# Performance work log

Hardware: AMD Instinct MI355X
Metric: run time of the kernel (lower is better)

The kernel has to match this reference:

```python
import jax, jax.numpy as jnp
import numpy as np

B, L = 1, 320
CS, CZ, CH, H, PQ, PV = 384, 128, 16, 12, 4, 8
INF, EPS = 1e5, 1e-8


def _quat_to_rot(q):
    w, x, y, z = q[..., 0], q[..., 1], q[..., 2], q[..., 3]
    r0 = jnp.stack([1 - 2*(y*y + z*z), 2*(x*y - w*z), 2*(x*z + w*y)], -1)
    r1 = jnp.stack([2*(x*y + w*z), 1 - 2*(x*x + z*z), 2*(y*z - w*x)], -1)
    r2 = jnp.stack([2*(x*z - w*y), 2*(y*z + w*x), 1 - 2*(x*x + y*y)], -1)
    return jnp.stack([r0, r1, r2], -2)


def setup_inputs():
    key = jax.random.key(0)
    ks = jax.random.split(key, 12)

    def lin(k, fan_in, fan_out):
        k1, k2 = jax.random.split(k)
        lim = 1.0 / np.sqrt(fan_in)
        return (jax.random.uniform(k1, (fan_in, fan_out), minval=-lim, maxval=lim, dtype=jnp.float32),
                jax.random.uniform(k2, (fan_out,), minval=-lim, maxval=lim, dtype=jnp.float32))

    s = jax.random.normal(ks[0], (B, L, CS), dtype=jnp.float32)
    quat = jax.random.normal(ks[1], (B, L, 4), dtype=jnp.float32)
    quat = quat / jnp.linalg.norm(quat, axis=-1, keepdims=True)
    rot = _quat_to_rot(quat)                                   # proper rotations (B,L,3,3)
    trans = 10.0 * jax.random.normal(ks[2], (B, L, 3), dtype=jnp.float32)
    z = jax.random.normal(ks[3], (B, L, L, CZ), dtype=jnp.float32)
    frame_mask = jnp.ones((B, L), dtype=jnp.float32)

    Wq, bq = lin(ks[4], CS, CH * H)
    Wkv, bkv = lin(ks[5], CS, 2 * CH * H)
    Wqp, bqp = lin(ks[6], CS, 6 * H * PQ)
    Wkvp, bkvp = lin(ks[7], CS, 6 * H * (PQ + PV))
    Wg, bg = lin(ks[8], CS, H * PQ)
    geom_weights = jnp.ones((3,), jnp.float32)
    dir_weight = jnp.asarray(0.5, jnp.float32)
    head_weights = 0.02 * jax.random.normal(ks[9], (H,), dtype=jnp.float32)
    concat_dim = H * (CH + 7 * PV) + H * CZ                    # 2400
    Wo, bo = lin(ks[10], concat_dim, CS)
    return dict(s=s, rot=rot, trans=trans, z=z, frame_mask=frame_mask,
                Wq=Wq, bq=bq, Wkv=Wkv, bkv=bkv, Wqp=Wqp, bqp=bqp,
                Wkvp=Wkvp, bkvp=bkvp, Wg=Wg, bg=bg,
                geom_weights=geom_weights, dir_weight=dir_weight,
                head_weights=head_weights, Wo=Wo, bo=bo)


def reference(s, rot, trans, z, frame_mask, Wq, bq, Wkv, bkv, Wqp, bqp,
              Wkvp, bkvp, Wg, bg, geom_weights, dir_weight, head_weights, Wo, bo):
    def proc_pts(pts_flat, P):
        # (B,L,6*H*P) -> rotate coords+translate, rotate dirs -> (B,L,H,P,6)
        pts = pts_flat.reshape(B, L, H, P, 6)
        coords = jnp.einsum('blij,blhpj->blhpi', rot, pts[..., :3]) + trans[:, :, None, None, :]
        dirs = jnp.einsum('blij,blhpj->blhpi', rot, pts[..., 3:])
        return jnp.concatenate([coords, dirs], -1)

    q = (s @ Wq + bq).reshape(B, L, H, CH)
    kv = s @ Wkv + bkv
    k = kv[..., :CH * H].reshape(B, L, H, CH)
    v = kv[..., CH * H:].reshape(B, L, H, CH)

    q_pts = proc_pts(s @ Wqp + bqp, PQ)
    kv_pts = s @ Wkvp + bkvp
    k_pts = proc_pts(kv_pts[..., :6 * H * PQ], PQ)
    v_pts = proc_pts(kv_pts[..., 6 * H * PQ:], PV)

    gate = jax.nn.sigmoid(s @ Wg + bg).reshape(B, L, H, PQ, 1)
    q_pts = q_pts * gate

    scalar_att = jnp.einsum('bqhc,bkhc->bhqk', q, k) / np.sqrt(CH).astype(np.float32)

    # position attention: per-pair point distances + log + inverse, mean over points
    delta = q_pts[:, :, None, :, :, :3] - k_pts[:, None, :, :, :, :3]   # (B,Lq,Lk,H,PQ,3)
    d = jnp.linalg.norm(delta, axis=-1)
    pos_att = (d + jnp.log(d + EPS) + 1.0 / (d + EPS)).mean(-1).transpose(0, 3, 1, 2)

    # direction attention: per-point dot minus cross-product 'curvature'
    qd, kd = q_pts[..., 3:], k_pts[..., 3:]
    dot = jnp.einsum('bqhpd,bkhpd->bqkhp', qd, kd)                       # (B,Lq,Lk,H,P)
    cr = jnp.cross(qd[:, :, None, :, None, :, :], kd[:, None, :, :, :, None, :])  # (B,Lq,Lk,H,Pk,Pq,3)
    cross = jnp.linalg.norm(cr, axis=-1).mean(-1)                        # (B,Lq,Lk,H,Pk)
    nq = jnp.linalg.norm(qd, axis=-1)[:, :, None]                        # (B,Lq,1,H,P)
    nk = jnp.linalg.norm(kd, axis=-1)[:, None]                           # (B,1,Lk,H,P)
    dir_att = (dot - cross / (nq * nk + EPS)).mean(-1).transpose(0, 3, 1, 2)

    att = scalar_att + dir_weight * (geom_weights[0] * pos_att + geom_weights[1] * dir_att)
    att = att * head_weights[:, None, None]
    mask2d = frame_mask[:, None, None, :] * frame_mask[:, None, :, None]  # (B,1,L,L)
    att = jax.nn.softmax(att + INF * (mask2d - 1.0), axis=-1)

    o_scalar = jnp.einsum('bhqk,bkhc->bqhc', att, v)
    o_geom = jnp.einsum('bhqk,bkhpd->bqhpd', att, v_pts)                 # (B,L,H,PV,6)

    # map aggregated geometry back into local frames
    rotT = jnp.swapaxes(rot, -1, -2)
    trans_inv = -jnp.einsum('blij,blj->bli', rotT, trans)
    lc = jnp.einsum('blij,blhpj->blhpi', rotT, o_geom[..., :3]) + trans_inv[:, :, None, None, :]
    ld = jnp.einsum('blij,blhpj->blhpi', rotT, o_geom[..., 3:6])
    ld = ld / jnp.maximum(jnp.linalg.norm(ld, axis=-1, keepdims=True), 1e-12)  # F.normalize
    ln = jnp.linalg.norm(lc, axis=-1, keepdims=True)
    o_geom7 = jnp.concatenate([lc, ld, ln], -1)                          # (B,L,H,PV,7)

    o_pair = jnp.einsum('bhij,bijk->bihk', att, z)                       # (B,L,H,CZ)
    out = jnp.concatenate([o_scalar.reshape(B, L, H * CH),
                           o_geom7.reshape(B, L, H * PV * 7),
                           o_pair.reshape(B, L, H * CZ)], -1)
    return out @ Wo + bo
```

## Files before the change

### kernel.cpp

```cpp
#include <hip/hip_runtime.h>
#include <hip/hip_bf16.h>
#include <math.h>

#define LSEQ 320
#define CS 384
#define CZ 128
#define CH 16
#define NH 12
#define PQ 4
#define PV 8
#define EPSF 1e-8f

typedef short short8 __attribute__((ext_vector_type(8)));
typedef float f32x4 __attribute__((ext_vector_type(4)));
typedef unsigned short ush2 __attribute__((ext_vector_type(2)));

__device__ __forceinline__ unsigned short f2b(float x) {
    union { float f; unsigned u; } v; v.f = x;
    unsigned r = (v.u + 0x7FFF + ((v.u >> 16) & 1)) >> 16;
    return (unsigned short)r;
}
__device__ __forceinline__ float b2f(unsigned short h) {
    union { unsigned u; float f; } v; v.u = ((unsigned)h) << 16;
    return v.f;
}

#define OFF_Q       0
#define OFF_KV      61440
#define OFF_QPT     184320
#define OFF_ATTHI   552960
#define OFF_ATTLO   1372160
#define OFF_CCHI    2191360
#define OFF_CCLO    2575360
#define OFF_SHI     2959360
#define OFF_SMID    2990080
#define OFF_SLO     3020800
#define OFF_WCATHI  3051520
#define OFF_WCATMID 3392512
#define OFF_WCATLO  3733504
#define OFF_BCAT    4074496
#define OFF_WOHI    4076272
#define OFF_WOLO    4537072
#define OFF_VKVHI   4997872
#define OFF_VKVLO   5120752
#define OFF_QPR     5243632
#define OFF_KVPR    5335792
#define OFF_GATE    5612272
#define OFF_PART    5627632
#define OFF_KROW    6242032

__global__ __launch_bounds__(256) void k_cast(
    const float* __restrict__ s,
    const float* __restrict__ Wq, const float* __restrict__ bq,
    const float* __restrict__ Wkv, const float* __restrict__ bkv,
    const float* __restrict__ Wqp, const float* __restrict__ bqp,
    const float* __restrict__ Wkvp, const float* __restrict__ bkvp,
    const float* __restrict__ Wg, const float* __restrict__ bg,
    const float* __restrict__ Wo,
    unsigned short* __restrict__ s_hi, unsigned short* __restrict__ s_mid,
    unsigned short* __restrict__ s_lo,
    unsigned short* __restrict__ w_hi, unsigned short* __restrict__ w_mid,
    unsigned short* __restrict__ w_lo,
    float* __restrict__ bcat,
    unsigned short* __restrict__ wo_hi, unsigned short* __restrict__ wo_lo,
    float* __restrict__ ph_hi, float* __restrict__ ph_lo)
{
    int i = blockIdx.x * 256 + threadIdx.x;
    if (i < 122880) {
        float x = s[i];
        unsigned short hi = f2b(x);
        float r1 = x - b2f(hi);
        unsigned short mid = f2b(r1);
        s_hi[i] = hi; s_mid[i] = mid; s_lo[i] = f2b(r1 - b2f(mid));
        return;
    }
    i -= 122880;
    if (i < 681984) {
        int k = i / 1776, c = i - k * 1776;
        float v;
        if (c < 192)       v = Wq[(size_t)k * 192 + c];
        else if (c < 576)  v = Wkv[(size_t)k * 384 + c - 192];
        else if (c < 864)  v = Wqp[(size_t)k * 288 + c - 576];
        else if (c < 1728) v = Wkvp[(size_t)k * 864 + c - 864];
        else               v = Wg[(size_t)k * 48 + c - 1728];
        unsigned short hi = f2b(v);
        float r1 = v - b2f(hi);
        unsigned short mid = f2b(r1);
        w_hi[i] = hi; w_mid[i] = mid; w_lo[i] = f2b(r1 - b2f(mid));
        return;
    }
    i -= 681984;
    if (i < 1776) {
        float v;
        if (i < 192)       v = bq[i];
        else if (i < 576)  v = bkv[i - 192];
        else if (i < 864)  v = bqp[i - 576];
        else if (i < 1728) v = bkvp[i - 864];
        else               v = bg[i - 1728];
        bcat[i] = v;
        return;
    }
    i -= 1776;
    if (i < 921600) {
        float v = Wo[i];
        unsigned short hi = f2b(v);
        wo_hi[i] = hi; wo_lo[i] = f2b(v - b2f(hi));
        return;
    }
    i -= 921600;
    if (i < 204800) { ph_hi[i] = 0.0f; return; }
    i -= 204800;
    if (i < 204800) ph_lo[i] = 0.0f;
}

__global__ __launch_bounds__(256) void k_proj(
    const unsigned short* __restrict__ s_hi, const unsigned short* __restrict__ s_mid,
    const unsigned short* __restrict__ s_lo,
    const unsigned short* __restrict__ wc_hi, const unsigned short* __restrict__ wc_mid,
    const unsigned short* __restrict__ wc_lo,
    const float* __restrict__ bcat,
    float* __restrict__ qo, float* __restrict__ kvo,
    float* __restrict__ qpr, float* __restrict__ kvpr, float* __restrict__ gate)
{
    __shared__ unsigned short a_h[64][56], a_m[64][56], a_l[64][56];
    __shared__ unsigned short w_h[48][56], w_m[48][56], w_l[48][56];
    int col0 = blockIdx.x * 48, l0 = blockIdx.y * 64;
    int tid = threadIdx.x;
    int lane = tid & 63, w = tid >> 6;
    int ncol = lane & 15, blk = lane >> 4, mrow = (lane >> 4) * 4;

    float* dst; int nc, cbase; bool sig = false;
    if (col0 < 192)       { nc = 192; cbase = col0;        dst = qo;   }
    else if (col0 < 576)  { nc = 384; cbase = col0 - 192;  dst = kvo;  }
    else if (col0 < 864)  { nc = 288; cbase = col0 - 576;  dst = qpr;  }
    else if (col0 < 1728) { nc = 864; cbase = col0 - 864;  dst = kvpr; }
    else                  { nc = 48;  cbase = 0;           dst = gate; sig = true; }

    f32x4 acc[3] = {};
    for (int k0 = 0; k0 < 384; k0 += 32) {
        __syncthreads();
        {
            int row = tid >> 2, seg = tid & 3;
            size_t off = (size_t)(l0 + row) * 384 + k0 + seg * 8;
            *(short8*)&a_h[row][seg * 8] = *(const short8*)(s_hi + off);
            *(short8*)&a_m[row][seg * 8] = *(const short8*)(s_mid + off);
            *(short8*)&a_l[row][seg * 8] = *(const short8*)(s_lo + off);
        }
        if (tid < 96) {
            int kk = tid / 3, coff = (tid % 3) * 16;
            size_t off = (size_t)(k0 + kk) * 1776 + col0 + coff;
            short8 h0 = *(const short8*)(wc_hi + off);
            short8 h1 = *(const short8*)(wc_hi + off + 8);
            short8 m0 = *(const short8*)(wc_mid + off);
            short8 m1 = *(const short8*)(wc_mid + off + 8);
            short8 l0v = *(const short8*)(wc_lo + off);
            short8 l1v = *(const short8*)(wc_lo + off + 8);
            #pragma unroll
            for (int i = 0; i < 8; i++) {
                w_h[coff + i][kk]     = (unsigned short)h0[i];
                w_h[coff + 8 + i][kk] = (unsigned short)h1[i];
                w_m[coff + i][kk]     = (unsigned short)m0[i];
                w_m[coff + 8 + i][kk] = (unsigned short)m1[i];
                w_l[coff + i][kk]     = (unsigned short)l0v[i];
                w_l[coff + 8 + i][kk] = (unsigned short)l1v[i];
            }
        }
        __syncthreads();
        short8 afh = *(short8*)&a_h[w * 16 + ncol][blk * 8];
        short8 afm = *(short8*)&a_m[w * 16 + ncol][blk * 8];
        short8 afl = *(short8*)&a_l[w * 16 + ncol][blk * 8];
        #pragma unroll
        for (int s3 = 0; s3 < 3; s3++) {
            short8 bfh = *(short8*)&w_h[s3 * 16 + ncol][blk * 8];
            short8 bfm = *(short8*)&w_m[s3 * 16 + ncol][blk * 8];
            short8 bfl = *(short8*)&w_l[s3 * 16 + ncol][blk * 8];
            acc[s3] = __builtin_amdgcn_mfma_f32_16x16x32_bf16(afm, bfm, acc[s3], 0, 0, 0);
            acc[s3] = __builtin_amdgcn_mfma_f32_16x16x32_bf16(afh, bfl, acc[s3], 0, 0, 0);
            acc[s3] = __builtin_amdgcn_mfma_f32_16x16x32_bf16(afl, bfh, acc[s3], 0, 0, 0);
            acc[s3] = __builtin_amdgcn_mfma_f32_16x16x32_bf16(afh, bfm, acc[s3], 0, 0, 0);
            acc[s3] = __builtin_amdgcn_mfma_f32_16x16x32_bf16(afm, bfh, acc[s3], 0, 0, 0);
            acc[s3] = __builtin_amdgcn_mfma_f32_16x16x32_bf16(afh, bfh, acc[s3], 0, 0, 0);
        }
    }
    #pragma unroll
    for (int s3 = 0; s3 < 3; s3++) {
        float bv = bcat[col0 + s3 * 16 + ncol];
        int cloc = cbase + s3 * 16 + ncol;
        #pragma unroll
        for (int r = 0; r < 4; r++) {
            float v2 = acc[s3][r] + bv;
            if (sig) v2 = 1.0f / (1.0f + expf(-v2));
            dst[(size_t)(l0 + w * 16 + mrow + r) * nc + cloc] = v2;
        }
    }
}

__global__ __launch_bounds__(256) void k_points(
    const float* __restrict__ qpr, const float* __restrict__ kvpr, const float* __restrict__ gate,
    const float* __restrict__ rot, const float* __restrict__ trans,
    const float* __restrict__ kv,
    float* __restrict__ qpt, float* __restrict__ krow,
    unsigned short* __restrict__ vkv_hi, unsigned short* __restrict__ vkv_lo)
{
    __shared__ float vsh[96][6];
    __shared__ float kp_s[48][6];
    __shared__ float kn_s[48];
    int l = blockIdx.x, t = threadIdx.x;
    const float* R = rot + l * 9;
    float tx = trans[l * 3], ty = trans[l * 3 + 1], tz = trans[l * 3 + 2];
    if (t < 192) {
        const float* src; float g = 1.0f; float* dst = nullptr; int vj = -1, kj = -1;
        if (t < 48)      { src = qpr + (size_t)l * 288 + t * 6; g = gate[l * 48 + t]; dst = qpt + ((size_t)l * 48 + t) * 6; }
        else if (t < 96) { kj = t - 48; src = kvpr + (size_t)l * 864 + kj * 6; }
        else             { int j = t - 96; src = kvpr + (size_t)l * 864 + 288 + j * 6; vj = j; }
        float px = src[0], py = src[1], pz = src[2], ux = src[3], uy = src[4], uz = src[5];
        float c0 = R[0] * px + R[1] * py + R[2] * pz + tx;
        float c1 = R[3] * px + R[4] * py + R[5] * pz + ty;
        float c2 = R[6] * px + R[7] * py + R[8] * pz + tz;
        float d0 = R[0] * ux + R[1] * uy + R[2] * uz;
        float d1 = R[3] * ux + R[4] * uy + R[5] * uz;
        float d2 = R[6] * ux + R[7] * uy + R[8] * uz;
        if (vj >= 0) {
            vsh[vj][0] = c0; vsh[vj][1] = c1; vsh[vj][2] = c2;
            vsh[vj][3] = d0; vsh[vj][4] = d1; vsh[vj][5] = d2;
        } else if (kj >= 0) {
            kp_s[kj][0] = c0; kp_s[kj][1] = c1; kp_s[kj][2] = c2;
            kp_s[kj][3] = d0; kp_s[kj][4] = d1; kp_s[kj][5] = d2;
            kn_s[kj] = sqrtf(d0 * d0 + d1 * d1 + d2 * d2);
        } else {
            dst[0] = c0 * g; dst[1] = c1 * g; dst[2] = c2 * g;
            dst[3] = d0 * g; dst[4] = d1 * g; dst[5] = d2 * g;
        }
    }
    __syncthreads();
    #pragma unroll
    for (int e = 0; e < 3; e++) {
        int u = t * 3 + e;
        int h = u >> 6, n = u & 63;
        float val;
        if (n < 16) val = kv[(size_t)l * 384 + 192 + h * 16 + n];
        else        val = vsh[h * 8 + (n - 16) / 6][(n - 16) % 6];
        unsigned short hi = f2b(val);
        size_t idx = ((size_t)h * 64 + n) * 320 + l;
        vkv_hi[idx] = hi;
        vkv_lo[idx] = f2b(val - b2f(hi));
    }
    for (int idx = t; idx < 576; idx += 256) {
        int h = idx / 48, j = idx - h * 48;
        float v;
        if (j < 24)      v = kp_s[h * 4 + j / 6][j % 6];
        else if (j < 40) v = kv[(size_t)l * 384 + h * 16 + (j - 24)];
        else if (j < 44) v = kn_s[h * 4 + (j - 40)];
        else             v = 0.0f;
        krow[((size_t)h * 320 + l) * 48 + j] = v;
    }
}

__global__ __launch_bounds__(256) void k_att(
    const float* __restrict__ qb, const float* __restrict__ qpt,
    const float* __restrict__ krow,
    const float* __restrict__ fm, const float* __restrict__ gw,
    const float* __restrict__ dwp, const float* __restrict__ hwp,
    unsigned short* __restrict__ att_hi, unsigned short* __restrict__ att_lo)
{
    int tid = threadIdx.x;
    int w = tid >> 6, lane = tid & 63;
    int iq = blockIdx.x * 4 + w;
    int h = blockIdx.y;

    float qv[CH];
    #pragma unroll
    for (int c = 0; c < CH; c++) qv[c] = qb[(size_t)iq * 192 + h * CH + c];
    float qp[24];
    #pragma unroll
    for (int j = 0; j < 24; j++) qp[j] = qpt[(size_t)iq * 288 + h * 24 + j];
    float nq[PQ], nq2[PQ];
    #pragma unroll
    for (int p = 0; p < PQ; p++) {
        float x = qp[p * 6 + 3], y = qp[p * 6 + 4], zz = qp[p * 6 + 5];
        nq2[p] = x * x + y * y + zz * zz;
        nq[p] = sqrtf(nq2[p]);
    }
    float dwv = dwp[0], g0 = gw[0], g1 = gw[1], hwv = hwp[h];
    float fmi = fm[iq];

    float lg[5];
    #pragma unroll
    for (int r = 0; r < 5; r++) {
        int kk = r * 64 + lane;
        const float* row = krow + ((size_t)h * 320 + kk) * 48;

        float scalar = 0.f;
        #pragma unroll
        for (int c = 0; c < CH; c++) scalar += qv[c] * row[24 + c];
        scalar *= 0.25f;

        float pos = 0.f;
        #pragma unroll
        for (int p = 0; p < PQ; p++) {
            float dx = qp[p * 6] - row[p * 6];
            float dy = qp[p * 6 + 1] - row[p * 6 + 1];
            float dz = qp[p * 6 + 2] - row[p * 6 + 2];
            float d = __builtin_amdgcn_sqrtf(dx * dx + dy * dy + dz * dz);
            float de = d + EPSF;
            pos += d + __logf(de) + __builtin_amdgcn_rcpf(de);
        }
        pos *= 0.25f;

        float dir = 0.f;
        #pragma unroll
        for (int p = 0; p < PQ; p++) {
            float kx = row[p * 6 + 3], ky = row[p * 6 + 4], kz = row[p * 6 + 5];
            float nk = row[40 + p];
            float nk2 = nk * nk;
            float cm = 0.f, dself = 0.f;
            #pragma unroll
            for (int pq = 0; pq < PQ; pq++) {
                float dq = qp[pq * 6 + 3] * kx + qp[pq * 6 + 4] * ky + qp[pq * 6 + 5] * kz;
                if (pq == p) dself = dq;
                cm += __builtin_amdgcn_sqrtf(fmaxf(nq2[pq] * nk2 - dq * dq, 0.0f));
            }
            cm *= 0.25f;
            dir += dself - cm * __builtin_amdgcn_rcpf(nq[p] * nk + EPSF);
        }
        dir *= 0.25f;

        float logit = scalar + dwv * (g0 * pos + g1 * dir);
        logit *= hwv;
        logit += 100000.0f * (fmi * fm[kk] - 1.0f);
        lg[r] = logit;
    }

    float mx = lg[0];
    #pragma unroll
    for (int r = 1; r < 5; r++) mx = fmaxf(mx, lg[r]);
    for (int m = 32; m; m >>= 1) mx = fmaxf(mx, __shfl_xor(mx, m, 64));

    float e[5], sm = 0.f;
    #pragma unroll
    for (int r = 0; r < 5; r++) { e[r] = __expf(lg[r] - mx); sm += e[r]; }
    for (int m = 32; m; m >>= 1) sm += __shfl_xor(sm, m, 64);
    float inv = 1.0f / sm;
    #pragma unroll
    for (int r = 0; r < 5; r++) {
        float p = e[r] * inv;
        unsigned short hi = f2b(p);
        size_t idx = ((size_t)h * 320 + iq) * 320 + r * 64 + lane;
        att_hi[idx] = hi;
        att_lo[idx] = f2b(p - b2f(hi));
    }
}

__global__ __launch_bounds__(256) void k_sv(
    const unsigned short* __restrict__ att_hi, const unsigned short* __restrict__ att_lo,
    const unsigned short* __restrict__ vkv_hi, const unsigned short* __restrict__ vkv_lo,
    const float* __restrict__ rot, const float* __restrict__ trans,
    unsigned short* __restrict__ cc_hi, unsigned short* __restrict__ cc_lo)
{
    __shared__ unsigned short a_hi[16][56];
    __shared__ unsigned short a_lo[16][56];
    __shared__ unsigned short bt_hi[64][56];
    __shared__ unsigned short bt_lo[64][56];
    __shared__ float ogsh[16][49];
    int iq0 = blockIdx.x * 16, h = blockIdx.y;
    int tid = threadIdx.x;
    int lane = tid & 63, w = tid >> 6;
    int ncol = lane & 15, mrow = (lane >> 4) * 4, blk = lane >> 4;

    f32x4 acc = {};
    for (int k0 = 0; k0 < 320; k0 += 32) {
        __syncthreads();
        if (tid < 64) {
            int row = tid >> 2, seg = tid & 3;
            size_t off = ((size_t)h * 320 + iq0 + row) * 320 + k0 + seg * 8;
            *(short8*)&a_hi[row][seg * 8] = *(const short8*)(att_hi + off);
            *(short8*)&a_lo[row][seg * 8] = *(const short8*)(att_lo + off);
        }
        {
            int row = tid >> 2, seg = tid & 3;
            size_t off = ((size_t)h * 64 + row) * 320 + k0 + seg * 8;
            *(short8*)&bt_hi[row][seg * 8] = *(const short8*)(vkv_hi + off);
            *(short8*)&bt_lo[row][seg * 8] = *(const short8*)(vkv_lo + off);
        }
        __syncthreads();
        short8 afh = *(short8*)&a_hi[ncol][blk * 8];
        short8 afl = *(short8*)&a_lo[ncol][blk * 8];
        short8 bfh = *(short8*)&bt_hi[w * 16 + ncol][blk * 8];
        short8 bfl = *(short8*)&bt_lo[w * 16 + ncol][blk * 8];
        acc = __builtin_amdgcn_mfma_f32_16x16x32_bf16(afh, bfh, acc, 0, 0, 0);
        acc = __builtin_amdgcn_mfma_f32_16x16x32_bf16(afh, bfl, acc, 0, 0, 0);
        acc = __builtin_amdgcn_mfma_f32_16x16x32_bf16(afl, bfh, acc, 0, 0, 0);
    }
    {
        int n = w * 16 + ncol;
        #pragma unroll
        for (int r = 0; r < 4; r++) {
            int iq = iq0 + mrow + r;
            float v = acc[r];
            if (n < 16) {
                unsigned short hi = f2b(v);
                size_t idx = (size_t)iq * 2400 + h * 16 + n;
                cc_hi[idx] = hi;
                cc_lo[idx] = f2b(v - b2f(hi));
            } else {
                ogsh[mrow + r][n - 16] = v;
            }
        }
    }
    __syncthreads();
    if (tid < 128) {
        int iqr = tid >> 3, p = tid & 7;
        int l = iq0 + iqr;
        const float* R = rot + l * 9;
        float tx = trans[l * 3], ty = trans[l * 3 + 1], tz = trans[l * 3 + 2];
        const float* o = &ogsh[iqr][p * 6];
        float gx = o[0] - tx, gy = o[1] - ty, gz = o[2] - tz;
        float l0 = R[0] * gx + R[3] * gy + R[6] * gz;
        float l1 = R[1] * gx + R[4] * gy + R[7] * gz;
        float l2 = R[2] * gx + R[5] * gy + R[8] * gz;
        float dx = o[3], dy = o[4], dz = o[5];
        float e0 = R[0] * dx + R[3] * dy + R[6] * dz;
        float e1 = R[1] * dx + R[4] * dy + R[7] * dz;
        float e2 = R[2] * dx + R[5] * dy + R[8] * dz;
        float n = sqrtf(e0 * e0 + e1 * e1 + e2 * e2);
        float inv = 1.0f / fmaxf(n, 1e-12f);
        float ln = sqrtf(l0 * l0 + l1 * l1 + l2 * l2);
        float vals[7] = { l0, l1, l2, e0 * inv, e1 * inv, e2 * inv, ln };
        size_t base = (size_t)l * 2400 + 192 + (h * PV + p) * 7;
        #pragma unroll
        for (int j = 0; j < 7; j++) {
            unsigned short hi = f2b(vals[j]);
            cc_hi[base + j] = hi;
            cc_lo[base + j] = f2b(vals[j] - b2f(hi));
        }
    }
}

__global__ __launch_bounds__(256) void k_pair(
    const unsigned short* __restrict__ att_hi, const unsigned short* __restrict__ att_lo,
    const float* __restrict__ z,
    unsigned short* __restrict__ cc_hi, unsigned short* __restrict__ cc_lo)
{
    __shared__ unsigned short a_hi[16][56];
    __shared__ unsigned short a_lo[16][56];
    __shared__ unsigned short zt_sh[128][56];
    int iq = blockIdx.x;
    int tid = threadIdx.x;
    int lane = tid & 63, w = tid >> 6;
    int ncol = lane & 15, blk = lane >> 4, mrow = (lane >> 4) * 4;

    f32x4 acc[2] = {};
    for (int k0 = 0; k0 < 320; k0 += 32) {
        __syncthreads();
        if (tid < 64) {
            int row = tid >> 2, seg = tid & 3;
            size_t off = (size_t)row * 102400 + (size_t)iq * 320 + k0 + seg * 8;
            *(short8*)&a_hi[row][seg * 8] = *(const short8*)(att_hi + off);
            *(short8*)&a_lo[row][seg * 8] = *(const short8*)(att_lo + off);
        }
        {
            int kp2 = (tid >> 4) * 2;
            int cb = (tid & 15) * 8;
            const float* src0 = z + ((size_t)iq * 320 + k0 + kp2) * 128 + cb;
            float4 a0 = *(const float4*)(src0);
            float4 a1 = *(const float4*)(src0 + 4);
            float4 b0 = *(const float4*)(src0 + 128);
            float4 b1 = *(const float4*)(src0 + 132);
            float va[8] = {a0.x, a0.y, a0.z, a0.w, a1.x, a1.y, a1.z, a1.w};
            float vb[8] = {b0.x, b0.y, b0.z, b0.w, b1.x, b1.y, b1.z, b1.w};
            #pragma unroll
            for (int c = 0; c < 8; c++) {
                ush2 pr;
                pr[0] = f2b(va[c]);
                pr[1] = f2b(vb[c]);
                *(ush2*)&zt_sh[cb + c][kp2] = pr;
            }
        }
        __syncthreads();
        short8 afh = *(short8*)&a_hi[ncol][blk * 8];
        short8 afl = *(short8*)&a_lo[ncol][blk * 8];
        #pragma unroll
        for (int s2 = 0; s2 < 2; s2++) {
            short8 bf = *(short8*)&zt_sh[w * 32 + s2 * 16 + ncol][blk * 8];
            acc[s2] = __builtin_amdgcn_mfma_f32_16x16x32_bf16(afl, bf, acc[s2], 0, 0, 0);
            acc[s2] = __builtin_amdgcn_mfma_f32_16x16x32_bf16(afh, bf, acc[s2], 0, 0, 0);
        }
    }
    #pragma unroll
    for (int s2 = 0; s2 < 2; s2++) {
        int n = w * 32 + s2 * 16 + ncol;
        #pragma unroll
        for (int r = 0; r < 4; r++) {
            int h = mrow + r;
            if (h < 12) {
                float v = acc[s2][r];
                unsigned short hi = f2b(v);
                size_t idx = (size_t)iq * 2400 + 864 + h * 128 + n;
                cc_hi[idx] = hi;
                cc_lo[idx] = f2b(v - b2f(hi));
            }
        }
    }
}

__global__ __launch_bounds__(256) void k_gemm(
    const unsigned short* __restrict__ cc_hi, const unsigned short* __restrict__ cc_lo,
    const unsigned short* __restrict__ wo_hi, const unsigned short* __restrict__ wo_lo,
    float* __restrict__ part)
{
    __shared__ unsigned short a_hi[64][56];
    __shared__ unsigned short a_lo[64][56];
    __shared__ unsigned short w_hi[48][56];
    __shared__ unsigned short w_lo[48][56];
    int iq0 = blockIdx.x * 64, col0 = blockIdx.y * 48, ks = blockIdx.z;
    int tid = threadIdx.x;
    int lane = tid & 63, w = tid >> 6;
    int ncol = lane & 15, blk = lane >> 4, mrow = (lane >> 4) * 4;

    f32x4 acc[3] = {};
    for (int kc = 0; kc < 15; kc++) {
        int k0 = ks * 480 + kc * 32;
        __syncthreads();
        {
            int row = tid >> 2, seg = tid & 3;
            size_t off = (size_t)(iq0 + row) * 2400 + k0 + seg * 8;
            *(short8*)&a_hi[row][seg * 8] = *(const short8*)(cc_hi + off);
            *(short8*)&a_lo[row][seg * 8] = *(const short8*)(cc_lo + off);
        }
        if (tid < 96) {
            int kk = tid / 3, coff = (tid % 3) * 16;
            size_t off = (size_t)(k0 + kk) * 384 + col0 + coff;
            short8 h0 = *(const short8*)(wo_hi + off);
            short8 h1 = *(const short8*)(wo_hi + off + 8);
            short8 l0v = *(const short8*)(wo_lo + off);
            short8 l1v = *(const short8*)(wo_lo + off + 8);
            #pragma unroll
            for (int i = 0; i < 8; i++) {
                w_hi[coff + i][kk]     = (unsigned short)h0[i];
                w_hi[coff + 8 + i][kk] = (unsigned short)h1[i];
                w_lo[coff + i][kk]     = (unsigned short)l0v[i];
                w_lo[coff + 8 + i][kk] = (unsigned short)l1v[i];
            }
        }
        __syncthreads();
        short8 afh = *(short8*)&a_hi[w * 16 + ncol][blk * 8];
        short8 afl = *(short8*)&a_lo[w * 16 + ncol][blk * 8];
        #pragma unroll
        for (int s3 = 0; s3 < 3; s3++) {
            short8 bfh = *(short8*)&w_hi[s3 * 16 + ncol][blk * 8];
            short8 bfl = *(short8*)&w_lo[s3 * 16 + ncol][blk * 8];
            acc[s3] = __builtin_amdgcn_mfma_f32_16x16x32_bf16(afh, bfh, acc[s3], 0, 0, 0);
            acc[s3] = __builtin_amdgcn_mfma_f32_16x16x32_bf16(afh, bfl, acc[s3], 0, 0, 0);
            acc[s3] = __builtin_amdgcn_mfma_f32_16x16x32_bf16(afl, bfh, acc[s3], 0, 0, 0);
        }
    }
    #pragma unroll
    for (int s3 = 0; s3 < 3; s3++) {
        int cn = col0 + s3 * 16 + ncol;
        #pragma unroll
        for (int r = 0; r < 4; r++)
            part[((size_t)ks * 320 + iq0 + w * 16 + mrow + r) * 384 + cn] = acc[s3][r];
    }
}

__global__ __launch_bounds__(256) void k_reduce(
    const float* __restrict__ part, const float* __restrict__ bo, float* __restrict__ out)
{
    int i = blockIdx.x * 256 + threadIdx.x;
    float v = bo[i % CS];
    #pragma unroll
    for (int ks = 0; ks < 5; ks++) v += part[(size_t)ks * 122880 + i];
    out[i] = v;
}

extern "C" void kernel_launch(void* const* d_in, const int* in_sizes, int n_in,
                              void* d_out, int out_size, void* d_ws, size_t ws_size,
                              hipStream_t stream)
{
    const float* s     = (const float*)d_in[0];
    const float* rot   = (const float*)d_in[1];
    const float* trans = (const float*)d_in[2];
    const float* z     = (const float*)d_in[3];
    const float* fm    = (const float*)d_in[4];
    const float* Wq    = (const float*)d_in[5];
    const float* bq    = (const float*)d_in[6];
    const float* Wkv   = (const float*)d_in[7];
    const float* bkv   = (const float*)d_in[8];
    const float* Wqp   = (const float*)d_in[9];
    const float* bqp   = (const float*)d_in[10];
    const float* Wkvp  = (const float*)d_in[11];
    const float* bkvp  = (const float*)d_in[12];
    const float* Wg    = (const float*)d_in[13];
    const float* bg    = (const float*)d_in[14];
    const float* gw    = (const float*)d_in[15];
    const float* dw    = (const float*)d_in[16];
    const float* hw    = (const float*)d_in[17];
    const float* Wo    = (const float*)d_in[18];
    const float* bo    = (const float*)d_in[19];

    float* ws = (float*)d_ws;
    float*          q       = ws + OFF_Q;
    float*          kv      = ws + OFF_KV;
    float*          qpt     = ws + OFF_QPT;
    unsigned short* att_hi  = (unsigned short*)(ws + OFF_ATTHI);
    unsigned short* att_lo  = (unsigned short*)(ws + OFF_ATTLO);
    float*          ph_hi   = ws + OFF_ATTHI + 12 * 51200;
    float*          ph_lo   = ws + OFF_ATTLO + 12 * 51200;
    unsigned short* cc_hi   = (unsigned short*)(ws + OFF_CCHI);
    unsigned short* cc_lo   = (unsigned short*)(ws + OFF_CCLO);
    unsigned short* s_hi    = (unsigned short*)(ws + OFF_SHI);
    unsigned short* s_mid   = (unsigned short*)(ws + OFF_SMID);
    unsigned short* s_lo    = (unsigned short*)(ws + OFF_SLO);
    unsigned short* wc_hi   = (unsigned short*)(ws + OFF_WCATHI);
    unsigned short* wc_mid  = (unsigned short*)(ws + OFF_WCATMID);
    unsigned short* wc_lo   = (unsigned short*)(ws + OFF_WCATLO);
    float*          bcat    = ws + OFF_BCAT;
    unsigned short* wo_hi   = (unsigned short*)(ws + OFF_WOHI);
    unsigned short* wo_lo   = (unsigned short*)(ws + OFF_WOLO);
    unsigned short* vkv_hi  = (unsigned short*)(ws + OFF_VKVHI);
    unsigned short* vkv_lo  = (unsigned short*)(ws + OFF_VKVLO);
    float*          qpr     = ws + OFF_QPR;
    float*          kvpr    = ws + OFF_KVPR;
    float*          gate    = ws + OFF_GATE;
    float*          part    = ws + OFF_PART;
    float*          krow    = ws + OFF_KROW;
    float* out = (float*)d_out;

    k_cast<<<dim3(8352), dim3(256), 0, stream>>>(s, Wq, bq, Wkv, bkv, Wqp, bqp,
                                                 Wkvp, bkvp, Wg, bg, Wo,
                                                 s_hi, s_mid, s_lo, wc_hi, wc_mid, wc_lo,
                                                 bcat, wo_hi, wo_lo, ph_hi, ph_lo);
    k_proj<<<dim3(37, 5), dim3(256), 0, stream>>>(s_hi, s_mid, s_lo, wc_hi, wc_mid, wc_lo,
                                                  bcat, q, kv, qpr, kvpr, gate);
    k_points<<<dim3(LSEQ), dim3(256), 0, stream>>>(qpr, kvpr, gate, rot, trans, kv,
                                                   qpt, krow, vkv_hi, vkv_lo);
    k_att<<<dim3(80, NH), dim3(256), 0, stream>>>(q, qpt, krow, fm, gw, dw, hw,
                                                  att_hi, att_lo);
    k_sv<<<dim3(20, NH), dim3(256), 0, stream>>>(att_hi, att_lo, vkv_hi, vkv_lo,
                                                 rot, trans, cc_hi, cc_lo);
    k_pair<<<dim3(LSEQ), dim3(256), 0, stream>>>(att_hi, att_lo, z, cc_hi, cc_lo);
    k_gemm<<<dim3(5, 8, 5), dim3(256), 0, stream>>>(cc_hi, cc_lo, wo_hi, wo_lo, part);
    k_reduce<<<dim3(480), dim3(256), 0, stream>>>(part, bo, out);
}
```

Baseline: 219.1 us.

## Pre-transpose weights for vectorized LDS staging and merge sv/pair kernels

After: 216.7 us. No clear change (-1.1%).

```diff
diff --git a/kernel.cpp b/kernel.cpp
--- a/kernel.cpp
+++ b/kernel.cpp
@@ -48,6 +48,11 @@
 #define OFF_GATE    5612272
 #define OFF_PART    5627632
 #define OFF_KROW    6242032
+#define OFF_WCTHI   6426352
+#define OFF_WCTMID  6767344
+#define OFF_WCTLO   7108336
+#define OFF_WOTHI   7449328
+#define OFF_WOTLO   7910128
 
 __global__ __launch_bounds__(256) void k_cast(
     const float* __restrict__ s,
@@ -113,11 +118,45 @@
     if (i < 204800) ph_lo[i] = 0.0f;
 }
 
+__global__ __launch_bounds__(256) void k_tr(
+    const unsigned short* __restrict__ wc_hi, const unsigned short* __restrict__ wc_mid,
+    const unsigned short* __restrict__ wc_lo,
+    const unsigned short* __restrict__ wo_hi, const unsigned short* __restrict__ wo_lo,
+    unsigned short* __restrict__ wcT_hi, unsigned short* __restrict__ wcT_mid,
+    unsigned short* __restrict__ wcT_lo,
+    unsigned short* __restrict__ woT_hi, unsigned short* __restrict__ woT_lo)
+{
+    int m = blockIdx.z;
+    const unsigned short* in; unsigned short* outp; int R, C;
+    if (m == 0)      { in = wc_hi;  outp = wcT_hi;  R = 384;  C = 1776; }
+    else if (m == 1) { in = wc_mid; outp = wcT_mid; R = 384;  C = 1776; }
+    else if (m == 2) { in = wc_lo;  outp = wcT_lo;  R = 384;  C = 1776; }
+    else if (m == 3) { in = wo_hi;  outp = woT_hi;  R = 2400; C = 384;  }
+    else             { in = wo_lo;  outp = woT_lo;  R = 2400; C = 384;  }
+    int r0 = blockIdx.x * 64, c0 = blockIdx.y * 64;
+    if (r0 >= R || c0 >= C) return;
+    __shared__ unsigned short t[64][65];
+    int tid = threadIdx.x;
+    #pragma unroll
+    for (int rep = 0; rep < 16; rep++) {
+        int idx = rep * 256 + tid;
+        int i = idx >> 6, j = idx & 63;
+        if (r0 + i < R && c0 + j < C) t[i][j] = in[(size_t)(r0 + i) * C + c0 + j];
+    }
+    __syncthreads();
+    #pragma unroll
+    for (int rep = 0; rep < 16; rep++) {
+        int idx = rep * 256 + tid;
+        int i = idx >> 6, j = idx & 63;
+        if (c0 + i < C && r0 + j < R) outp[(size_t)(c0 + i) * R + r0 + j] = t[j][i];
+    }
+}
+
 __global__ __launch_bounds__(256) void k_proj(
     const unsigned short* __restrict__ s_hi, const unsigned short* __restrict__ s_mid,
     const unsigned short* __restrict__ s_lo,
-    const unsigned short* __restrict__ wc_hi, const unsigned short* __restrict__ wc_mid,
-    const unsigned short* __restrict__ wc_lo,
+    const unsigned short* __restrict__ wcT_hi, const unsigned short* __restrict__ wcT_mid,
+    const unsigned short* __restrict__ wcT_lo,
     const float* __restrict__ bcat,
     float* __restrict__ qo, float* __restrict__ kvo,
     float* __restrict__ qpr, float* __restrict__ kvpr, float* __restrict__ gate)
@@ -146,24 +185,12 @@
             *(short8*)&a_m[row][seg * 8] = *(const short8*)(s_mid + off);
             *(short8*)&a_l[row][seg * 8] = *(const short8*)(s_lo + off);
         }
-        if (tid < 96) {
-            int kk = tid / 3, coff = (tid % 3) * 16;
-            size_t off = (size_t)(k0 + kk) * 1776 + col0 + coff;
-            short8 h0 = *(const short8*)(wc_hi + off);
-            short8 h1 = *(const short8*)(wc_hi + off + 8);
-            short8 m0 = *(const short8*)(wc_mid + off);
-            short8 m1 = *(const short8*)(wc_mid + off + 8);
-            short8 l0v = *(const short8*)(wc_lo + off);
-            short8 l1v = *(const short8*)(wc_lo + off + 8);
-            #pragma unroll
-            for (int i = 0; i < 8; i++) {
-                w_h[coff + i][kk]     = (unsigned short)h0[i];
-                w_h[coff + 8 + i][kk] = (unsigned short)h1[i];
-                w_m[coff + i][kk]     = (unsigned short)m0[i];
-                w_m[coff + 8 + i][kk] = (unsigned short)m1[i];
-                w_l[coff + i][kk]     = (unsigned short)l0v[i];
-                w_l[coff + 8 + i][kk] = (unsigned short)l1v[i];
-            }
+        if (tid < 192) {
+            int row = tid >> 2, seg = tid & 3;
+            size_t off = (size_t)(col0 + row) * 384 + k0 + seg * 8;
+            *(short8*)&w_h[row][seg * 8] = *(const short8*)(wcT_hi + off);
+            *(short8*)&w_m[row][seg * 8] = *(const short8*)(wcT_mid + off);
+            *(short8*)&w_l[row][seg * 8] = *(const short8*)(wcT_lo + off);
         }
         __syncthreads();
         short8 afh = *(short8*)&a_h[w * 16 + ncol][blk * 8];
@@ -351,153 +378,143 @@
     }
 }
 
-__global__ __launch_bounds__(256) void k_sv(
+__global__ __launch_bounds__(256) void k_svpair(
     const unsigned short* __restrict__ att_hi, const unsigned short* __restrict__ att_lo,
     const unsigned short* __restrict__ vkv_hi, const unsigned short* __restrict__ vkv_lo,
+    const float* __restrict__ z,
     const float* __restrict__ rot, const float* __restrict__ trans,
     unsigned short* __restrict__ cc_hi, unsigned short* __restrict__ cc_lo)
 {
     __shared__ unsigned short a_hi[16][56];
     __shared__ unsigned short a_lo[16][56];
-    __shared__ unsigned short bt_hi[64][56];
-    __shared__ unsigned short bt_lo[64][56];
+    __shared__ unsigned short B[128][56];
     __shared__ float ogsh[16][49];
-    int iq0 = blockIdx.x * 16, h = blockIdx.y;
-    int tid = threadIdx.x;
-    int lane = tid & 63, w = tid >> 6;
-    int ncol = lane & 15, mrow = (lane >> 4) * 4, blk = lane >> 4;
-
-    f32x4 acc = {};
-    for (int k0 = 0; k0 < 320; k0 += 32) {
-        __syncthreads();
-        if (tid < 64) {
-            int row = tid >> 2, seg = tid & 3;
-            size_t off = ((size_t)h * 320 + iq0 + row) * 320 + k0 + seg * 8;
-            *(short8*)&a_hi[row][seg * 8] = *(const short8*)(att_hi + off);
-            *(short8*)&a_lo[row][seg * 8] = *(const short8*)(att_lo + off);
-        }
-        {
-            int row = tid >> 2, seg = tid & 3;
-            size_t off = ((size_t)h * 64 + row) * 320 + k0 + seg * 8;
-            *(short8*)&bt_hi[row][seg * 8] = *(const short8*)(vkv_hi + off);
-            *(short8*)&bt_lo[row][seg * 8] = *(const short8*)(vkv_lo + off);
-        }
-        __syncthreads();
-        short8 afh = *(short8*)&a_hi[ncol][blk * 8];
-        short8 afl = *(short8*)&a_lo[ncol][blk * 8];
-        short8 bfh = *(short8*)&bt_hi[w * 16 + ncol][blk * 8];
-        short8 bfl = *(short8*)&bt_lo[w * 16 + ncol][blk * 8];
-        acc = __builtin_amdgcn_mfma_f32_16x16x32_bf16(afh, bfh, acc, 0, 0, 0);
-        acc = __builtin_amdgcn_mfma_f32_16x16x32_bf16(afh, bfl, acc, 0, 0, 0);
-        acc = __builtin_amdgcn_mfma_f32_16x16x32_bf16(afl, bfh, acc, 0, 0, 0);
-    }
-    {
-        int n = w * 16 + ncol;
-        #pragma unroll
-        for (int r = 0; r < 4; r++) {
-            int iq = iq0 + mrow + r;
-            float v = acc[r];
-            if (n < 16) {
-                unsigned short hi = f2b(v);
-                size_t idx = (size_t)iq * 2400 + h * 16 + n;
-                cc_hi[idx] = hi;
-                cc_lo[idx] = f2b(v - b2f(hi));
-            } else {
-                ogsh[mrow + r][n - 16] = v;
-            }
-        }
-    }
-    __syncthreads();
-    if (tid < 128) {
-        int iqr = tid >> 3, p = tid & 7;
-        int l = iq0 + iqr;
-        const float* R = rot + l * 9;
-        float tx = trans[l * 3], ty = trans[l * 3 + 1], tz = trans[l * 3 + 2];
-        const float* o = &ogsh[iqr][p * 6];
-        float gx = o[0] - tx, gy = o[1] - ty, gz = o[2] - tz;
-        float l0 = R[0] * gx + R[3] * gy + R[6] * gz;
-        float l1 = R[1] * gx + R[4] * gy + R[7] * gz;
-        float l2 = R[2] * gx + R[5] * gy + R[8] * gz;
-        float dx = o[3], dy = o[4], dz = o[5];
-        float e0 = R[0] * dx + R[3] * dy + R[6] * dz;
-        float e1 = R[1] * dx + R[4] * dy + R[7] * dz;
-        float e2 = R[2] * dx + R[5] * dy + R[8] * dz;
-        float n = sqrtf(e0 * e0 + e1 * e1 + e2 * e2);
-        float inv = 1.0f / fmaxf(n, 1e-12f);
-        float ln = sqrtf(l0 * l0 + l1 * l1 + l2 * l2);
-        float vals[7] = { l0, l1, l2, e0 * inv, e1 * inv, e2 * inv, ln };
-        size_t base = (size_t)l * 2400 + 192 + (h * PV + p) * 7;
-        #pragma unroll
-        for (int j = 0; j < 7; j++) {
-            unsigned short hi = f2b(vals[j]);
-            cc_hi[base + j] = hi;
-            cc_lo[base + j] = f2b(vals[j] - b2f(hi));
-        }
-    }
-}
-
-__global__ __launch_bounds__(256) void k_pair(
-    const unsigned short* __restrict__ att_hi, const unsigned short* __restrict__ att_lo,
-    const float* __restrict__ z,
-    unsigned short* __restrict__ cc_hi, unsigned short* __restrict__ cc_lo)
-{
-    __shared__ unsigned short a_hi[16][56];
-    __shared__ unsigned short a_lo[16][56];
-    __shared__ unsigned short zt_sh[128][56];
-    int iq = blockIdx.x;
+    int bid = blockIdx.x;
     int tid = threadIdx.x;
     int lane = tid & 63, w = tid >> 6;
     int ncol = lane & 15, blk = lane >> 4, mrow = (lane >> 4) * 4;
 
-    f32x4 acc[2] = {};
-    for (int k0 = 0; k0 < 320; k0 += 32) {
+    if (bid < 240) {
+        int iq0 = (bid % 20) * 16, h = bid / 20;
+        f32x4 acc = {};
+        for (int k0 = 0; k0 < 320; k0 += 32) {
+            __syncthreads();
+            if (tid < 64) {
+                int row = tid >> 2, seg = tid & 3;
+                size_t off = ((size_t)h * 320 + iq0 + row) * 320 + k0 + seg * 8;
+                *(short8*)&a_hi[row][seg * 8] = *(const short8*)(att_hi + off);
+                *(short8*)&a_lo[row][seg * 8] = *(const short8*)(att_lo + off);
+            }
+            {
+                int row = tid >> 2, seg = tid & 3;
+                size_t off = ((size_t)h * 64 + row) * 320 + k0 + seg * 8;
+                *(short8*)&B[row][seg * 8]      = *(const short8*)(vkv_hi + off);
+                *(short8*)&B[64 + row][seg * 8] = *(const short8*)(vkv_lo + off);
+            }
+            __syncthreads();
+            short8 afh = *(short8*)&a_hi[ncol][blk * 8];
+            short8 afl = *(short8*)&a_lo[ncol][blk * 8];
+            short8 bfh = *(short8*)&B[w * 16 + ncol][blk * 8];
+            short8 bfl = *(short8*)&B[64 + w * 16 + ncol][blk * 8];
+            acc = __builtin_amdgcn_mfma_f32_16x16x32_bf16(afh, bfh, acc, 0, 0, 0);
+            acc = __builtin_amdgcn_mfma_f32_16x16x32_bf16(afh, bfl, acc, 0, 0, 0);
+            acc = __builtin_amdgcn_mfma_f32_16x16x32_bf16(afl, bfh, acc, 0, 0, 0);
+        }
+        {
+            int n = w * 16 + ncol;
+            #pragma unroll
+            for (int r = 0; r < 4; r++) {
+                int iq = iq0 + mrow + r;
+                float v = acc[r];
+                if (n < 16) {
+                    unsigned short hi = f2b(v);
+                    size_t idx = (size_t)iq * 2400 + h * 16 + n;
+                    cc_hi[idx] = hi;
+                    cc_lo[idx] = f2b(v - b2f(hi));
+                } else {
+                    ogsh[mrow + r][n - 16] = v;
+                }
+            }
+        }
         __syncthreads();
-        if (tid < 64) {
-            int row = tid >> 2, seg = tid & 3;
-            size_t off = (size_t)row * 102400 + (size_t)iq * 320 + k0 + seg * 8;
-            *(short8*)&a_hi[row][seg * 8] = *(const short8*)(att_hi + off);
-            *(short8*)&a_lo[row][seg * 8] = *(const short8*)(att_lo + off);
-        }
-        {
-            int kp2 = (tid >> 4) * 2;
-            int cb = (tid & 15) * 8;
-            const float* src0 = z + ((size_t)iq * 320 + k0 + kp2) * 128 + cb;
-            float4 a0 = *(const float4*)(src0);
-            float4 a1 = *(const float4*)(src0 + 4);
-            float4 b0 = *(const float4*)(src0 + 128);
-            float4 b1 = *(const float4*)(src0 + 132);
-            float va[8] = {a0.x, a0.y, a0.z, a0.w, a1.x, a1.y, a1.z, a1.w};
-            float vb[8] = {b0.x, b0.y, b0.z, b0.w, b1.x, b1.y, b1.z, b1.w};
+        if (tid < 128) {
+            int iqr = tid >> 3, p = tid & 7;
+            int l = iq0 + iqr;
+            const float* R = rot + l * 9;
+            float tx = trans[l * 3], ty = trans[l * 3 + 1], tz = trans[l * 3 + 2];
+            const float* o = &ogsh[iqr][p * 6];
+            float gx = o[0] - tx, gy = o[1] - ty, gz = o[2] - tz;
+            float l0 = R[0] * gx + R[3] * gy + R[6] * gz;
+            float l1 = R[1] * gx + R[4] * gy + R[7] * gz;
+            float l2 = R[2] * gx + R[5] * gy + R[8] * gz;
+            float dx = o[3], dy = o[4], dz = o[5];
+            float e0 = R[0] * dx + R[3] * dy + R[6] * dz;
+            float e1 = R[1] * dx + R[4] * dy + R[7] * dz;
+            float e2 = R[2] * dx + R[5] * dy + R[8] * dz;
+            float n = sqrtf(e0 * e0 + e1 * e1 + e2 * e2);
+            float inv = 1.0f / fmaxf(n, 1e-12f);
+            float ln = sqrtf(l0 * l0 + l1 * l1 + l2 * l2);
+            float vals[7] = { l0, l1, l2, e0 * inv, e1 * inv, e2 * inv, ln };
+            size_t base = (size_t)l * 2400 + 192 + (h * PV + p) * 7;
             #pragma unroll
-            for (int c = 0; c < 8; c++) {
-                ush2 pr;
-                pr[0] = f2b(va[c]);
-                pr[1] = f2b(vb[c]);
-                *(ush2*)&zt_sh[cb + c][kp2] = pr;
-            }
-        }
-        __syncthreads();
-        short8 afh = *(short8*)&a_hi[ncol][blk * 8];
-        short8 afl = *(short8*)&a_lo[ncol][blk * 8];
+            for (int j = 0; j < 7; j++) {
+                unsigned short hi = f2b(vals[j]);
+                cc_hi[base + j] = hi;
+                cc_lo[base + j] = f2b(vals[j] - b2f(hi));
+            }
+        }
+    } else {
+        int iq = bid - 240;
+        f32x4 acc[2] = {};
+        for (int k0 = 0; k0 < 320; k0 += 32) {
+            __syncthreads();
+            if (tid < 64) {
+                int row = tid >> 2, seg = tid & 3;
+                size_t off = (size_t)row * 102400 + (size_t)iq * 320 + k0 + seg * 8;
+                *(short8*)&a_hi[row][seg * 8] = *(const short8*)(att_hi + off);
+                *(short8*)&a_lo[row][seg * 8] = *(const short8*)(att_lo + off);
+            }
+            {
+                int kp2 = (tid >> 4) * 2;
+                int cb = (tid & 15) * 8;
+                const float* src0 = z + ((size_t)iq * 320 + k0 + kp2) * 128 + cb;
+                float4 a0 = *(const float4*)(src0);
+                float4 a1 = *(const float4*)(src0 + 4);
+                float4 b0 = *(const float4*)(src0 + 128);
+                float4 b1 = *(const float4*)(src0 + 132);
+                float va[8] = {a0.x, a0.y, a0.z, a0.w, a1.x, a1.y, a1.z, a1.w};
+                float vb[8] = {b0.x, b0.y, b0.z, b0.w, b1.x, b1.y, b1.z, b1.w};
+                #pragma unroll
+                for (int c = 0; c < 8; c++) {
+                    ush2 pr;
+                    pr[0] = f2b(va[c]);
+                    pr[1] = f2b(vb[c]);
+                    *(ush2*)&B[cb + c][kp2] = pr;
+                }
+            }
+            __syncthreads();
+            short8 afh = *(short8*)&a_hi[ncol][blk * 8];
+            short8 afl = *(short8*)&a_lo[ncol][blk * 8];
+            #pragma unroll
+            for (int s2 = 0; s2 < 2; s2++) {
+                short8 bf = *(short8*)&B[w * 32 + s2 * 16 + ncol][blk * 8];
+                acc[s2] = __builtin_amdgcn_mfma_f32_16x16x32_bf16(afl, bf, acc[s2], 0, 0, 0);
+                acc[s2] = __builtin_amdgcn_mfma_f32_16x16x32_bf16(afh, bf, acc[s2], 0, 0, 0);
+            }
+        }
         #pragma unroll
         for (int s2 = 0; s2 < 2; s2++) {
-            short8 bf = *(short8*)&zt_sh[w * 32 + s2 * 16 + ncol][blk * 8];
-            acc[s2] = __builtin_amdgcn_mfma_f32_16x16x32_bf16(afl, bf, acc[s2], 0, 0, 0);
-            acc[s2] = __builtin_amdgcn_mfma_f32_16x16x32_bf16(afh, bf, acc[s2], 0, 0, 0);
-        }
-    }
-    #pragma unroll
-    for (int s2 = 0; s2 < 2; s2++) {
-        int n = w * 32 + s2 * 16 + ncol;
-        #pragma unroll
-        for (int r = 0; r < 4; r++) {
-            int h = mrow + r;
-            if (h < 12) {
-                float v = acc[s2][r];
-                unsigned short hi = f2b(v);
-                size_t idx = (size_t)iq * 2400 + 864 + h * 128 + n;
-                cc_hi[idx] = hi;
-                cc_lo[idx] = f2b(v - b2f(hi));
+            int n = w * 32 + s2 * 16 + ncol;
+            #pragma unroll
+            for (int r = 0; r < 4; r++) {
+                int h = mrow + r;
+                if (h < 12) {
+                    float v = acc[s2][r];
+                    unsigned short hi = f2b(v);
+                    size_t idx = (size_t)iq * 2400 + 864 + h * 128 + n;
+                    cc_hi[idx] = hi;
+                    cc_lo[idx] = f2b(v - b2f(hi));
+                }
             }
         }
     }
@@ -505,7 +522,7 @@
 
 __global__ __launch_bounds__(256) void k_gemm(
     const unsigned short* __restrict__ cc_hi, const unsigned short* __restrict__ cc_lo,
-    const unsigned short* __restrict__ wo_hi, const unsigned short* __restrict__ wo_lo,
+    const unsigned short* __restrict__ woT_hi, const unsigned short* __restrict__ woT_lo,
     float* __restrict__ part)
 {
     __shared__ unsigned short a_hi[64][56];
@@ -527,20 +544,11 @@
             *(short8*)&a_hi[row][seg * 8] = *(const short8*)(cc_hi + off);
             *(short8*)&a_lo[row][seg * 8] = *(const short8*)(cc_lo + off);
         }
-        if (tid < 96) {
-            int kk = tid / 3, coff = (tid % 3) * 16;
-            size_t off = (size_t)(k0 + kk) * 384 + col0 + coff;
-            short8 h0 = *(const short8*)(wo_hi + off);
-            short8 h1 = *(const short8*)(wo_hi + off + 8);
-            short8 l0v = *(const short8*)(wo_lo + off);
-            short8 l1v = *(const short8*)(wo_lo + off + 8);
-            #pragma unroll
-            for (int i = 0; i < 8; i++) {
-                w_hi[coff + i][kk]     = (unsigned short)h0[i];
-                w_hi[coff + 8 + i][kk] = (unsigned short)h1[i];
-                w_lo[coff + i][kk]     = (unsigned short)l0v[i];
-                w_lo[coff + 8 + i][kk] = (unsigned short)l1v[i];
-            }
+        if (tid < 192) {
+            int row = tid >> 2, seg = tid & 3;
+            size_t off = (size_t)(col0 + row) * 2400 + k0 + seg * 8;
+            *(short8*)&w_hi[row][seg * 8] = *(const short8*)(woT_hi + off);
+            *(short8*)&w_lo[row][seg * 8] = *(const short8*)(woT_lo + off);
         }
         __syncthreads();
         short8 afh = *(short8*)&a_hi[w * 16 + ncol][blk * 8];
@@ -624,21 +632,27 @@
     float*          gate    = ws + OFF_GATE;
     float*          part    = ws + OFF_PART;
     float*          krow    = ws + OFF_KROW;
+    unsigned short* wcT_hi  = (unsigned short*)(ws + OFF_WCTHI);
+    unsigned short* wcT_mid = (unsigned short*)(ws + OFF_WCTMID);
+    unsigned short* wcT_lo  = (unsigned short*)(ws + OFF_WCTLO);
+    unsigned short* woT_hi  = (unsigned short*)(ws + OFF_WOTHI);
+    unsigned short* woT_lo  = (unsigned short*)(ws + OFF_WOTLO);
     float* out = (float*)d_out;
 
     k_cast<<<dim3(8352), dim3(256), 0, stream>>>(s, Wq, bq, Wkv, bkv, Wqp, bqp,
                                                  Wkvp, bkvp, Wg, bg, Wo,
                                                  s_hi, s_mid, s_lo, wc_hi, wc_mid, wc_lo,
                                                  bcat, wo_hi, wo_lo, ph_hi, ph_lo);
-    k_proj<<<dim3(37, 5), dim3(256), 0, stream>>>(s_hi, s_mid, s_lo, wc_hi, wc_mid, wc_lo,
+    k_tr<<<dim3(38, 28, 5), dim3(256), 0, stream>>>(wc_hi, wc_mid, wc_lo, wo_hi, wo_lo,
+                                                    wcT_hi, wcT_mid, wcT_lo, woT_hi, woT_lo);
+    k_proj<<<dim3(37, 5), dim3(256), 0, stream>>>(s_hi, s_mid, s_lo, wcT_hi, wcT_mid, wcT_lo,
                                                   bcat, q, kv, qpr, kvpr, gate);
     k_points<<<dim3(LSEQ), dim3(256), 0, stream>>>(qpr, kvpr, gate, rot, trans, kv,
                                                    qpt, krow, vkv_hi, vkv_lo);
     k_att<<<dim3(80, NH), dim3(256), 0, stream>>>(q, qpt, krow, fm, gw, dw, hw,
                                                   att_hi, att_lo);
-    k_sv<<<dim3(20, NH), dim3(256), 0, stream>>>(att_hi, att_lo, vkv_hi, vkv_lo,
-                                                 rot, trans, cc_hi, cc_lo);
-    k_pair<<<dim3(LSEQ), dim3(256), 0, stream>>>(att_hi, att_lo, z, cc_hi, cc_lo);
-    k_gemm<<<dim3(5, 8, 5), dim3(256), 0, stream>>>(cc_hi, cc_lo, wo_hi, wo_lo, part);
+    k_svpair<<<dim3(560), dim3(256), 0, stream>>>(att_hi, att_lo, vkv_hi, vkv_lo, z,
+                                                  rot, trans, cc_hi, cc_lo);
+    k_gemm<<<dim3(5, 8, 5), dim3(256), 0, stream>>>(cc_hi, cc_lo, woT_hi, woT_lo, part);
     k_reduce<<<dim3(480), dim3(256), 0, stream>>>(part, bo, out);
 }
```
